# Performance work log

Measured on AMD Instinct MI355X. Metric: run time of the kernel, lower is better.

## Reference

```python
import jax, jax.numpy as jnp
import numpy as np

B, L, F = 256, 1800, 50
E, K, H, D = 4, 2, 32, 64
MAXH, HU = 900, 32


def setup_inputs() -> dict:
    key = jax.random.key(0)
    ks = jax.random.split(key, 24)
    s = 0.1
    nrm = lambda k, shape: jax.random.normal(k, shape, jnp.float32) * s
    return {
        "x": jax.random.normal(ks[0], (B, L, F), jnp.float32),
        "horizon": jax.random.randint(ks[1], (B,), 0, MAXH + 1),
        "W_in": nrm(ks[2], (D, F)), "b_in": nrm(ks[3], (D,)),
        "emb": nrm(ks[4], (MAXH + 1, D)),
        "W_gate": nrm(ks[5], (E, D)), "b_gate": nrm(ks[6], (E,)),
        "Wih0": nrm(ks[7], (E, 3 * H, D)), "Whh0": nrm(ks[8], (E, 3 * H, H)),
        "bih0": nrm(ks[9], (E, 3 * H)), "bhh0": nrm(ks[10], (E, 3 * H)),
        "Wih1": nrm(ks[11], (E, 3 * H, H)), "Whh1": nrm(ks[12], (E, 3 * H, H)),
        "bih1": nrm(ks[13], (E, 3 * H)), "bhh1": nrm(ks[14], (E, 3 * H)),
        "Wh1": nrm(ks[15], (E, HU, H)), "bh1": nrm(ks[16], (E, HU)),
        "Wh2": nrm(ks[17], (E, 1, HU)), "bh2": nrm(ks[18], (E, 1)),
    }


def _gru_layer(x_seq, Wih, Whh, bih, bhh):
    # x_seq: (L, B, Din). PyTorch GRU cell math (gate order r, z, n).
    xg = jnp.einsum('lbd,gd->lbg', x_seq, Wih) + bih  # (L, B, 3H)
    h0 = jnp.zeros((x_seq.shape[1], H), x_seq.dtype)

    def step(h, xgt):
        gh = h @ Whh.T + bhh
        r = jax.nn.sigmoid(xgt[:, :H] + gh[:, :H])
        z = jax.nn.sigmoid(xgt[:, H:2 * H] + gh[:, H:2 * H])
        n = jnp.tanh(xgt[:, 2 * H:] + r * gh[:, 2 * H:])
        h_new = (1.0 - z) * n + z * h
        return h_new, h_new

    h_last, hs = jax.lax.scan(step, h0, xg)
    return h_last, hs


def _expert(x_seq, Wih0, Whh0, bih0, bhh0, Wih1, Whh1, bih1, bhh1, Wh1, bh1, Wh2, bh2):
    _, hs0 = _gru_layer(x_seq, Wih0, Whh0, bih0, bhh0)      # layer 0: full sequence
    h1, _ = _gru_layer(hs0, Wih1, Whh1, bih1, bhh1)          # layer 1: final hidden (B, H)
    hid = jax.nn.relu(h1 @ Wh1.T + bh1)                      # head MLP (eval: dropout = id)
    return (hid @ Wh2.T + bh2)[:, 0]                         # (B,)


def reference(x, horizon, W_in, b_in, emb, W_gate, b_gate,
              Wih0, Whh0, bih0, bhh0, Wih1, Whh1, bih1, bhh1,
              Wh1, bh1, Wh2, bh2):
    x_proj = jnp.einsum('blf,df->bld', x, W_in) + b_in       # input_proj
    h_embed = emb[horizon]                                   # (B, D)
    x_proj = x_proj + h_embed[:, None, :]
    gate_logits = h_embed @ W_gate.T + b_gate                # (B, E)
    topk_logits, topk_idx = jax.lax.top_k(gate_logits, K)
    topk_w = jax.nn.softmax(topk_logits, axis=-1)
    Bn = x.shape[0]
    # dense routing weights (B, E): zero for non-routed experts -> identical math
    w_dense = jnp.zeros((Bn, E), x.dtype).at[jnp.arange(Bn)[:, None], topk_idx].add(topk_w)
    x_seq = jnp.transpose(x_proj, (1, 0, 2))                 # (L, B, D)
    preds = jax.vmap(_expert, in_axes=(None,) + (0,) * 12)(
        x_seq, Wih0, Whh0, bih0, bhh0, Wih1, Whh1, bih1, bhh1, Wh1, bh1, Wh2, bh2)  # (E, B)
    return jnp.sum(w_dense.T * preds, axis=0)                # (B,)
```

## Files before the change

kernel.cpp:

```cpp
#include <hip/hip_runtime.h>
#include <math.h>

#define NB   256
#define LSEQ 1800
#define NF   50
#define NE   4
#define NH   32
#define G3   96
#define ND   64
#define NHU  32
#define CHUNK 72
#define TBLK  8
#define NCHUNK (LSEQ / CHUNK)
#define NBLK   (CHUNK / TBLK)

typedef float v2f __attribute__((ext_vector_type(2)));

__device__ __forceinline__ v2f v2fma(v2f a, v2f b, v2f c) {
    return __builtin_elementwise_fma(a, b, c);
}
__device__ __forceinline__ v2f mkv2(float a, float b) { v2f t; t.x = a; t.y = b; return t; }
__device__ __forceinline__ v2f splat2(float s) { v2f t; t.x = s; t.y = s; return t; }

__device__ __forceinline__ float xor32sum(float v) {
    float t = v, u = v;
    asm("v_permlane32_swap_b32 %0, %1" : "+v"(t), "+v"(u));
    return t + u;
}

__global__ void compute_C_kernel(const float* __restrict__ Wih0,
                                 const float* __restrict__ W_in,
                                 float* __restrict__ Cg) {
    int e = blockIdx.x;
    for (int idx = threadIdx.x; idx < NF * G3; idx += blockDim.x) {
        int f = idx / G3;
        int g = idx - f * G3;
        const float* wr = Wih0 + ((size_t)e * G3 + g) * ND;
        float s = 0.f;
        #pragma unroll 8
        for (int d = 0; d < ND; d++) s += wr[d] * W_in[d * NF + f];
        Cg[(size_t)e * NF * G3 + idx] = s;
    }
}

__device__ __forceinline__ float fsig(float x) {
    float e = __builtin_amdgcn_exp2f(-1.442695041f * x);
    return __builtin_amdgcn_rcpf(1.f + e);
}
__device__ __forceinline__ float ftanh(float x) {
    x = fmaxf(x, -20.f);
    float e = __builtin_amdgcn_exp2f(-2.885390082f * x);
    return (1.f - e) * __builtin_amdgcn_rcpf(1.f + e);
}

__global__ __launch_bounds__(64, 1)
void moe_gru_kernel(const float* __restrict__ x,
                    const int*   __restrict__ horizon,
                    const float* __restrict__ emb,
                    const float* __restrict__ W_gate,
                    const float* __restrict__ b_gate,
                    const float* __restrict__ b_in,
                    const float* __restrict__ Wih0,
                    const float* __restrict__ Whh0,
                    const float* __restrict__ bih0,
                    const float* __restrict__ bhh0,
                    const float* __restrict__ Wih1,
                    const float* __restrict__ Whh1,
                    const float* __restrict__ bih1,
                    const float* __restrict__ bhh1,
                    const float* __restrict__ Wh1,
                    const float* __restrict__ bh1,
                    const float* __restrict__ Wh2,
                    const float* __restrict__ bh2,
                    const float* __restrict__ Cg,
                    float* __restrict__ out) {
    __shared__ __align__(16) float smem[4800 + 3600 + 64 + 64 + 32];
    float* CT  = smem;
    float* xs  = smem + 4800;
    float* heL = smem + 4800 + 3600;
    float* bbL = heL + 64;
    float* h1L = bbL + 64;

    const int bid = blockIdx.x;
    const int b   = bid >> 2;
    const int e   = bid & 3;
    const int tid = threadIdx.x;
    const int j   = tid & 31;
    const int hlf = tid >> 5;
    const int k0h = hlf << 4;

    {
        int hor = horizon[b];
        float he = emb[(size_t)hor * ND + tid];
        heL[tid] = he;
        bbL[tid] = he + b_in[tid];
    }

    float lg[NE];
    #pragma unroll
    for (int q = 0; q < NE; q++) {
        float s = b_gate[q];
        for (int d = 0; d < ND; d++) s += heL[d] * W_gate[q * ND + d];
        lg[q] = s;
    }
    int i1 = 0;
    #pragma unroll
    for (int q = 1; q < NE; q++) if (lg[q] > lg[i1]) i1 = q;
    int i2 = (i1 == 0) ? 1 : 0;
    #pragma unroll
    for (int q = 0; q < NE; q++) if (q != i1 && lg[q] > lg[i2]) i2 = q;
    if (e != i1 && e != i2) return;
    const float ex2 = expf(lg[i2] - lg[i1]);
    const float wgt = (e == i1) ? (1.f / (1.f + ex2)) : (ex2 / (1.f + ex2));

    for (int idx = tid; idx < NF * G3; idx += 64)
        CT[idx] = Cg[(size_t)e * NF * G3 + idx];

    v2f sA0[16], sA1[16], sA2[16];
    v2f wB0[8], wB1[8], wB2[8];
    {
        const float* baseA = (hlf ? Wih1 : Whh0) + (size_t)e * G3 * NH;
        const float* rA0 = baseA + (size_t)j * NH;
        const float* rA1 = baseA + (size_t)(j + 32) * NH;
        const float* rA2 = baseA + (size_t)(j + 64) * NH;
        #pragma unroll
        for (int q4 = 0; q4 < 8; q4++) {
            float4 qa = ((const float4*)rA0)[q4];
            sA0[2*q4] = mkv2(qa.x, qa.y); sA0[2*q4+1] = mkv2(qa.z, qa.w);
            float4 qb = ((const float4*)rA1)[q4];
            sA1[2*q4] = mkv2(qb.x, qb.y); sA1[2*q4+1] = mkv2(qb.z, qb.w);
            float4 qc = ((const float4*)rA2)[q4];
            sA2[2*q4] = mkv2(qc.x, qc.y); sA2[2*q4+1] = mkv2(qc.z, qc.w);
        }
        const float* baseB = Whh1 + (size_t)e * G3 * NH;
        const float* rB0 = baseB + (size_t)j * NH + k0h;
        const float* rB1 = baseB + (size_t)(j + 32) * NH + k0h;
        const float* rB2 = baseB + (size_t)(j + 64) * NH + k0h;
        #pragma unroll
        for (int q4 = 0; q4 < 4; q4++) {
            float4 qa = ((const float4*)rB0)[q4];
            wB0[2*q4] = mkv2(qa.x, qa.y); wB0[2*q4+1] = mkv2(qa.z, qa.w);
            float4 qb = ((const float4*)rB1)[q4];
            wB1[2*q4] = mkv2(qb.x, qb.y); wB1[2*q4+1] = mkv2(qb.z, qb.w);
            float4 qc = ((const float4*)rB2)[q4];
            wB2[2*q4] = mkv2(qc.x, qc.y); wB2[2*q4+1] = mkv2(qc.z, qc.w);
        }
    }
    const float selb0 = hlf ? bih1[e*G3 + j]      : bhh0[e*G3 + j];
    const float selb1 = hlf ? bih1[e*G3 + j + 32] : bhh0[e*G3 + j + 32];
    const float selb2 = hlf ? bih1[e*G3 + j + 64] : bhh0[e*G3 + j + 64];
    const float whb0  = hlf ? 0.f : bhh1[e*G3 + j];
    const float whb1  = hlf ? 0.f : bhh1[e*G3 + j + 32];
    const float whb2  = hlf ? 0.f : bhh1[e*G3 + j + 64];

    float dreg0, dreg1, dreg2;
    {
        float s0 = bih0[e*G3 + j], s1 = bih0[e*G3 + j + 32], s2 = bih0[e*G3 + j + 64];
        const float* w0 = Wih0 + ((size_t)e * G3 + j) * ND;
        const float* w1 = Wih0 + ((size_t)e * G3 + j + 32) * ND;
        const float* w2 = Wih0 + ((size_t)e * G3 + j + 64) * ND;
        for (int d = 0; d < ND; d++) {
            float bb = bbL[d];
            s0 += w0[d] * bb; s1 += w1[d] * bb; s2 += w2[d] * bb;
        }
        dreg0 = hlf ? 0.f : s0;
        dreg1 = hlf ? 0.f : s1;
        dreg2 = hlf ? 0.f : s2;
    }

    v2f h0v[16], h1v[8];
    #pragma unroll
    for (int k = 0; k < 16; k++) h0v[k] = splat2(0.f);
    #pragma unroll
    for (int k = 0; k < 8; k++)  h1v[k] = splat2(0.f);
    float hold = 0.f;
    float lmul = hlf ? 0.f : 1.f;
    if (tid < 32) h1L[tid] = 0.f;

    const float* xg = x + (size_t)b * LSEQ * NF;

    for (int ch = 0; ch < NCHUNK; ch++) {
        {
            const float4* xc4 = (const float4*)(xg + (size_t)ch * CHUNK * NF);
            float4 vb[7];
            #pragma unroll
            for (int u = 0; u < 7; u++) vb[u] = xc4[tid + 64 * u];
            #pragma unroll
            for (int u = 0; u < 7; u++) {
                int idx = (tid + 64 * u) * 4;
                #pragma unroll
                for (int uu = 0; uu < 4; uu++) {
                    int id = idx + uu;
                    int it = (int)(((unsigned)id * 5243u) >> 18);
                    int f  = id - it * 50;
                    float val = (uu == 0) ? vb[u].x : (uu == 1) ? vb[u].y
                              : (uu == 2) ? vb[u].z : vb[u].w;
                    xs[f * CHUNK + it] = val;
                }
            }
            #pragma unroll
            for (int u = 0; u < 7; u++) vb[u] = xc4[tid + 64 * (u + 7)];
            #pragma unroll
            for (int u = 0; u < 7; u++) {
                int idx = (tid + 64 * (u + 7)) * 4;
                #pragma unroll
                for (int uu = 0; uu < 4; uu++) {
                    int id = idx + uu;
                    int it = (int)(((unsigned)id * 5243u) >> 18);
                    int f  = id - it * 50;
                    float val = (uu == 0) ? vb[u].x : (uu == 1) ? vb[u].y
                              : (uu == 2) ? vb[u].z : vb[u].w;
                    xs[f * CHUNK + it] = val;
                }
            }
            if (tid < 4) {
                float4 v = xc4[896 + tid];
                int idx = (896 + tid) * 4;
                #pragma unroll
                for (int uu = 0; uu < 4; uu++) {
                    int id = idx + uu;
                    int it = (int)(((unsigned)id * 5243u) >> 18);
                    int f  = id - it * 50;
                    float val = (uu == 0) ? v.x : (uu == 1) ? v.y
                              : (uu == 2) ? v.z : v.w;
                    xs[f * CHUNK + it] = val;
                }
            }
        }

        for (int blk = 0; blk < NBLK; blk++) {
            const int ib0 = blk * TBLK;
            v2f a0[4], a1[4], a2[4];
            #pragma unroll
            for (int p = 0; p < 4; p++) {
                a0[p] = splat2(dreg0); a1[p] = splat2(dreg1); a2[p] = splat2(dreg2);
            }
            {
                const int fb = 25 * hlf;
                #pragma unroll 5
                for (int f = 0; f < 25; f++) {
                    const int fg = fb + f;
                    float c0 = CT[fg * G3 + j];
                    float c1 = CT[fg * G3 + j + 32];
                    float c2 = CT[fg * G3 + j + 64];
                    const float4* xp = (const float4*)(xs + fg * CHUNK + ib0);
                    float4 xa = xp[0], xb = xp[1];
                    v2f xv[4] = { mkv2(xa.x, xa.y), mkv2(xa.z, xa.w),
                                  mkv2(xb.x, xb.y), mkv2(xb.z, xb.w) };
                    v2f w0 = splat2(c0), w1 = splat2(c1), w2 = splat2(c2);
                    #pragma unroll
                    for (int p = 0; p < 4; p++) {
                        a0[p] = v2fma(w0, xv[p], a0[p]);
                        a1[p] = v2fma(w1, xv[p], a1[p]);
                        a2[p] = v2fma(w2, xv[p], a2[p]);
                    }
                }
            }
            #pragma unroll
            for (int p = 0; p < 4; p++) {
                a0[p].x = xor32sum(a0[p].x); a0[p].y = xor32sum(a0[p].y);
                a1[p].x = xor32sum(a1[p].x); a1[p].y = xor32sum(a1[p].y);
                a2[p].x = xor32sum(a2[p].x); a2[p].y = xor32sum(a2[p].y);
            }

            #pragma unroll
            for (int i = 0; i < TBLK; i++) {
                v2f dA0 = mkv2(selb0, 0.f), dA1 = mkv2(selb1, 0.f), dA2 = mkv2(selb2, 0.f);
                #pragma unroll
                for (int k = 0; k < 16; k++) {
                    dA0 = v2fma(sA0[k], h0v[k], dA0);
                    dA1 = v2fma(sA1[k], h0v[k], dA1);
                    dA2 = v2fma(sA2[k], h0v[k], dA2);
                }
                float A0 = dA0.x + dA0.y, A1 = dA1.x + dA1.y, A2 = dA2.x + dA2.y;
                v2f dB0 = mkv2(whb0, 0.f), dB1 = mkv2(whb1, 0.f), dB2 = mkv2(whb2, 0.f);
                #pragma unroll
                for (int k = 0; k < 8; k++) {
                    dB0 = v2fma(wB0[k], h1v[k], dB0);
                    dB1 = v2fma(wB1[k], h1v[k], dB1);
                    dB2 = v2fma(wB2[k], h1v[k], dB2);
                }
                float R0 = xor32sum(dB0.x + dB0.y);
                float R1 = xor32sum(dB1.x + dB1.y);
                float R2 = xor32sum(dB2.x + dB2.y);
                const float ac0 = a0[i >> 1][i & 1];
                const float ac1 = a1[i >> 1][i & 1];
                const float ac2 = a2[i >> 1][i & 1];
                float o0   = hlf ? R0 : ac0;
                float o1   = hlf ? R1 : ac1;
                float npre = hlf ? A2 : ac2;
                float gn   = hlf ? R2 : A2;
                float r = fsig(A0 + o0);
                float z = fsig(A1 + o1);
                float n = ftanh(npre + r * gn);
                float hnew = (n + z * (hold - n)) * lmul;
                hold = hnew;
                lmul = 1.f;
                if (hlf) h1L[j] = hnew;
                const float4* h1q = (const float4*)(h1L + k0h);
                float4 q0 = h1q[0], q1 = h1q[1], q2 = h1q[2], q3 = h1q[3];
                h1v[0] = mkv2(q0.x, q0.y); h1v[1] = mkv2(q0.z, q0.w);
                h1v[2] = mkv2(q1.x, q1.y); h1v[3] = mkv2(q1.z, q1.w);
                h1v[4] = mkv2(q2.x, q2.y); h1v[5] = mkv2(q2.z, q2.w);
                h1v[6] = mkv2(q3.x, q3.y); h1v[7] = mkv2(q3.z, q3.w);
                {
                    int hni = __float_as_int(hnew);
                    #pragma unroll
                    for (int k = 0; k < 16; k++) {
                        float e0 = __int_as_float(__builtin_amdgcn_readlane(hni, 2*k));
                        float e1 = __int_as_float(__builtin_amdgcn_readlane(hni, 2*k+1));
                        h0v[k] = mkv2(e0, e1);
                    }
                }
            }
        }
    }

    {
        v2f dA0 = mkv2(selb0, 0.f), dA1 = mkv2(selb1, 0.f), dA2 = mkv2(selb2, 0.f);
        #pragma unroll
        for (int k = 0; k < 16; k++) {
            dA0 = v2fma(sA0[k], h0v[k], dA0);
            dA1 = v2fma(sA1[k], h0v[k], dA1);
            dA2 = v2fma(sA2[k], h0v[k], dA2);
        }
        v2f dB0 = mkv2(whb0, 0.f), dB1 = mkv2(whb1, 0.f), dB2 = mkv2(whb2, 0.f);
        #pragma unroll
        for (int k = 0; k < 8; k++) {
            dB0 = v2fma(wB0[k], h1v[k], dB0);
            dB1 = v2fma(wB1[k], h1v[k], dB1);
            dB2 = v2fma(wB2[k], h1v[k], dB2);
        }
        float A0 = dA0.x + dA0.y, A1 = dA1.x + dA1.y, A2 = dA2.x + dA2.y;
        float R0 = xor32sum(dB0.x + dB0.y);
        float R1 = xor32sum(dB1.x + dB1.y);
        float R2 = xor32sum(dB2.x + dB2.y);
        float r = fsig(A0 + R0);
        float z = fsig(A1 + R1);
        float n = ftanh(A2 + r * R2);
        float hfin = n + z * (hold - n);
        if (hlf) h1L[j] = hfin;
    }

    if (tid < 32) {
        float s = bh1[e * NHU + tid];
        const float* wr = Wh1 + ((size_t)e * NHU + tid) * NH;
        #pragma unroll
        for (int d = 0; d < NH; d++) s += wr[d] * h1L[d];
        float hid = fmaxf(s, 0.f);
        float c = hid * Wh2[e * NHU + tid];
        #pragma unroll
        for (int off = 16; off > 0; off >>= 1) c += __shfl_down(c, off, 64);
        if (tid == 0) atomicAdd(out + b, wgt * (c + bh2[e]));
    }
}

extern "C" void kernel_launch(void* const* d_in, const int* in_sizes, int n_in,
                              void* d_out, int out_size, void* d_ws, size_t ws_size,
                              hipStream_t stream) {
    const float* x       = (const float*)d_in[0];
    const int*   horizon = (const int*)  d_in[1];
    const float* W_in    = (const float*)d_in[2];
    const float* b_in    = (const float*)d_in[3];
    const float* emb     = (const float*)d_in[4];
    const float* W_gate  = (const float*)d_in[5];
    const float* b_gate  = (const float*)d_in[6];
    const float* Wih0    = (const float*)d_in[7];
    const float* Whh0    = (const float*)d_in[8];
    const float* bih0    = (const float*)d_in[9];
    const float* bhh0    = (const float*)d_in[10];
    const float* Wih1    = (const float*)d_in[11];
    const float* Whh1    = (const float*)d_in[12];
    const float* bih1    = (const float*)d_in[13];
    const float* bhh1    = (const float*)d_in[14];
    const float* Wh1     = (const float*)d_in[15];
    const float* bh1     = (const float*)d_in[16];
    const float* Wh2     = (const float*)d_in[17];
    const float* bh2     = (const float*)d_in[18];
    float* out = (float*)d_out;
    float* Cg  = (float*)d_ws;

    hipMemsetAsync(d_out, 0, NB * sizeof(float), stream);
    compute_C_kernel<<<dim3(NE), dim3(256), 0, stream>>>(Wih0, W_in, Cg);
    moe_gru_kernel<<<dim3(NB * NE), dim3(64), 0, stream>>>(
        x, horizon, emb, W_gate, b_gate, b_in,
        Wih0, Whh0, bih0, bhh0, Wih1, Whh1, bih1, bhh1,
        Wh1, bh1, Wh2, bh2, Cg, out);
}
```

Measured before the change: 1.222 ms.

## Software-pipeline input projection of next time block into recurrent steps

```diff
diff --git a/kernel.cpp b/kernel.cpp
--- a/kernel.cpp
+++ b/kernel.cpp
@@ -88,6 +88,7 @@
     const int j   = tid & 31;
     const int hlf = tid >> 5;
     const int k0h = hlf << 4;
+    const int fb  = 25 * hlf;
 
     {
         int hor = horizon[b];
@@ -177,6 +178,9 @@
     float lmul = hlf ? 0.f : 1.f;
     if (tid < 32) h1L[tid] = 0.f;
 
+    v2f aP0[4], aP1[4], aP2[4];
+    constexpr int FS[TBLK + 1] = {0, 3, 6, 9, 12, 15, 18, 21, 25};
+
     const float* xg = x + (size_t)b * LSEQ * NF;
 
     for (int ch = 0; ch < NCHUNK; ch++) {
@@ -228,43 +232,67 @@
             }
         }
 
+        {
+            #pragma unroll
+            for (int p = 0; p < 4; p++) {
+                aP0[p] = splat2(dreg0); aP1[p] = splat2(dreg1); aP2[p] = splat2(dreg2);
+            }
+            #pragma unroll 5
+            for (int f = 0; f < 25; f++) {
+                const int fg = fb + f;
+                float c0 = CT[fg * G3 + j];
+                float c1 = CT[fg * G3 + j + 32];
+                float c2 = CT[fg * G3 + j + 64];
+                const float4* xp = (const float4*)(xs + fg * CHUNK);
+                float4 xa = xp[0], xb = xp[1];
+                v2f xv[4] = { mkv2(xa.x, xa.y), mkv2(xa.z, xa.w),
+                              mkv2(xb.x, xb.y), mkv2(xb.z, xb.w) };
+                v2f w0 = splat2(c0), w1 = splat2(c1), w2 = splat2(c2);
+                #pragma unroll
+                for (int p = 0; p < 4; p++) {
+                    aP0[p] = v2fma(w0, xv[p], aP0[p]);
+                    aP1[p] = v2fma(w1, xv[p], aP1[p]);
+                    aP2[p] = v2fma(w2, xv[p], aP2[p]);
+                }
+            }
+            #pragma unroll
+            for (int p = 0; p < 4; p++) {
+                aP0[p].x = xor32sum(aP0[p].x); aP0[p].y = xor32sum(aP0[p].y);
+                aP1[p].x = xor32sum(aP1[p].x); aP1[p].y = xor32sum(aP1[p].y);
+                aP2[p].x = xor32sum(aP2[p].x); aP2[p].y = xor32sum(aP2[p].y);
+            }
+        }
+
         for (int blk = 0; blk < NBLK; blk++) {
-            const int ib0 = blk * TBLK;
-            v2f a0[4], a1[4], a2[4];
-            #pragma unroll
-            for (int p = 0; p < 4; p++) {
-                a0[p] = splat2(dreg0); a1[p] = splat2(dreg1); a2[p] = splat2(dreg2);
-            }
-            {
-                const int fb = 25 * hlf;
-                #pragma unroll 5
-                for (int f = 0; f < 25; f++) {
+            const int ib0n = (blk + 1) * TBLK;
+            v2f aN0[4], aN1[4], aN2[4];
+
+            #pragma unroll
+            for (int i = 0; i < TBLK; i++) {
+                if (i == 0) {
+                    #pragma unroll
+                    for (int p = 0; p < 4; p++) {
+                        aN0[p] = splat2(dreg0); aN1[p] = splat2(dreg1); aN2[p] = splat2(dreg2);
+                    }
+                }
+                #pragma unroll
+                for (int f = FS[i]; f < FS[i + 1]; f++) {
                     const int fg = fb + f;
                     float c0 = CT[fg * G3 + j];
                     float c1 = CT[fg * G3 + j + 32];
                     float c2 = CT[fg * G3 + j + 64];
-                    const float4* xp = (const float4*)(xs + fg * CHUNK + ib0);
+                    const float4* xp = (const float4*)(xs + fg * CHUNK + ib0n);
                     float4 xa = xp[0], xb = xp[1];
                     v2f xv[4] = { mkv2(xa.x, xa.y), mkv2(xa.z, xa.w),
                                   mkv2(xb.x, xb.y), mkv2(xb.z, xb.w) };
                     v2f w0 = splat2(c0), w1 = splat2(c1), w2 = splat2(c2);
                     #pragma unroll
                     for (int p = 0; p < 4; p++) {
-                        a0[p] = v2fma(w0, xv[p], a0[p]);
-                        a1[p] = v2fma(w1, xv[p], a1[p]);
-                        a2[p] = v2fma(w2, xv[p], a2[p]);
+                        aN0[p] = v2fma(w0, xv[p], aN0[p]);
+                        aN1[p] = v2fma(w1, xv[p], aN1[p]);
+                        aN2[p] = v2fma(w2, xv[p], aN2[p]);
                     }
                 }
-            }
-            #pragma unroll
-            for (int p = 0; p < 4; p++) {
-                a0[p].x = xor32sum(a0[p].x); a0[p].y = xor32sum(a0[p].y);
-                a1[p].x = xor32sum(a1[p].x); a1[p].y = xor32sum(a1[p].y);
-                a2[p].x = xor32sum(a2[p].x); a2[p].y = xor32sum(a2[p].y);
-            }
-
-            #pragma unroll
-            for (int i = 0; i < TBLK; i++) {
                 v2f dA0 = mkv2(selb0, 0.f), dA1 = mkv2(selb1, 0.f), dA2 = mkv2(selb2, 0.f);
                 #pragma unroll
                 for (int k = 0; k < 16; k++) {
@@ -283,9 +311,9 @@
                 float R0 = xor32sum(dB0.x + dB0.y);
                 float R1 = xor32sum(dB1.x + dB1.y);
                 float R2 = xor32sum(dB2.x + dB2.y);
-                const float ac0 = a0[i >> 1][i & 1];
-                const float ac1 = a1[i >> 1][i & 1];
-                const float ac2 = a2[i >> 1][i & 1];
+                const float ac0 = aP0[i >> 1][i & 1];
+                const float ac1 = aP1[i >> 1][i & 1];
+                const float ac2 = aP2[i >> 1][i & 1];
                 float o0   = hlf ? R0 : ac0;
                 float o1   = hlf ? R1 : ac1;
                 float npre = hlf ? A2 : ac2;
@@ -313,6 +341,13 @@
                     }
                 }
             }
+
+            #pragma unroll
+            for (int p = 0; p < 4; p++) {
+                aP0[p].x = xor32sum(aN0[p].x); aP0[p].y = xor32sum(aN0[p].y);
+                aP1[p].x = xor32sum(aN1[p].x); aP1[p].y = xor32sum(aN1[p].y);
+                aP2[p].x = xor32sum(aN2[p].x); aP2[p].y = xor32sum(aN2[p].y);
+            }
         }
     }
 
```

Measured after the change: 1.853 ms. 1.52x slower.
